# Kernel tuning notes

Measured on AMD Instinct MI355X. Metric: run time of the kernel, lower is better.

The kernel has to match this reference:

```python
import jax, jax.numpy as jnp
import numpy as np

B, T, D = 2, 4096, 512
H = 8  # heads; head_dim = D // H = 64


def setup_inputs() -> dict:
    key = jax.random.key(0)
    ks = jax.random.split(key, 8)
    s = 0.02
    return {
        "queries": jax.random.normal(ks[0], (B, T, D), jnp.float32),
        "keys": jax.random.normal(ks[1], (B, T, D), jnp.float32),
        "values": jax.random.normal(ks[2], (B, T, D), jnp.float32),
        "Wq": jax.random.normal(ks[3], (D, D), jnp.float32) * s,
        "Wk": jax.random.normal(ks[4], (D, D), jnp.float32) * s,
        "Wv": jax.random.normal(ks[5], (D, D), jnp.float32) * s,
        "Wo": jax.random.normal(ks[6], (D, D), jnp.float32) * s,
        "bo": jnp.zeros((D,), jnp.float32),
    }


def reference(queries, keys, values, Wq, Wk, Wv, Wo, bo):
    # pad_dim = 0 for in_dim=512, n_heads=8, so no padding needed.
    Bq, Tq, _ = queries.shape
    Ts = keys.shape[1]
    hd = D // H
    # torch Linear: x @ W.T
    q = (queries @ Wq.T).reshape(Bq, Tq, H, hd).transpose(0, 2, 1, 3)  # [B,H,T,hd]
    k = (keys @ Wk.T).reshape(Bq, Ts, H, hd).transpose(0, 2, 1, 3)
    v = (values @ Wv.T).reshape(Bq, Ts, H, hd).transpose(0, 2, 1, 3)
    attn = jnp.einsum("bhtd,bhsd->bhts", q, k) / np.sqrt(hd).astype(np.float32)
    attn = jax.nn.softmax(attn, axis=-1)  # [B,H,T,Ts]
    z = jnp.einsum("bhts,bhsd->bhtd", attn, v)
    z = z.transpose(0, 2, 1, 3).reshape(Bq, Tq, D)
    out = z @ Wo.T + bo
    return (out, attn)
```

## Files before the change

### kernel.cpp

```cpp
#include <hip/hip_runtime.h>

typedef __attribute__((ext_vector_type(8))) short bf16x8;
typedef __attribute__((ext_vector_type(8))) unsigned short u16x8;
typedef __attribute__((ext_vector_type(4))) float f32x4;
typedef __attribute__((ext_vector_type(2))) unsigned uint2v;
typedef __attribute__((ext_vector_type(4))) unsigned uint4v;

#define DEVINL __device__ __forceinline__

constexpr int TB = 2;
constexpr int TT = 4096;
constexpr int TD = 512;
constexpr int TH = 8;
constexpr int THD = 64;
constexpr int TM = TB * TT;

DEVINL unsigned short f2b(float f) {
  unsigned u = __builtin_bit_cast(unsigned, f);
  u += 0x7FFFu + ((u >> 16) & 1u);
  return (unsigned short)(u >> 16);
}

DEVINL unsigned cvtpk(float lo, float hi) {
  unsigned r;
  asm("v_cvt_pk_bf16_f32 %0, %1, %2" : "=v"(r) : "v"(lo), "v"(hi));
  return r;
}

DEVINL void lgkm_barrier() {
  asm volatile("s_waitcnt lgkmcnt(0)" ::: "memory");
  __builtin_amdgcn_s_barrier();
  __builtin_amdgcn_sched_barrier(0);
}

__global__ __launch_bounds__(256, 2)
void proj_qkv(const float* __restrict__ Xq, const float* __restrict__ Xk,
              const float* __restrict__ Xv, const float* __restrict__ Wq,
              const float* __restrict__ Wk, const float* __restrict__ Wv,
              unsigned short* __restrict__ qb, unsigned short* __restrict__ kb,
              unsigned short* __restrict__ vt)
{
  constexpr int K = TD, N = TD;
  __shared__ unsigned short As[128][72];
  __shared__ unsigned short Bs[128][72];

  const int z = blockIdx.z;
  const float* X = (z == 0) ? Xq : (z == 1) ? Xk : Xv;
  const float* W = (z == 0) ? Wq : (z == 1) ? Wk : Wv;
  unsigned short* Yb = (z == 0) ? qb : (z == 1) ? kb : vt;
  const bool TR = (z == 2);

  const int t    = threadIdx.x;
  const int lane = t & 63, w = t >> 6;
  const int fr = lane & 15, fq = lane >> 4;
  const int wr = (w >> 1) * 64, wc = (w & 1) * 64;
  const int bm = blockIdx.x * 128, bn = blockIdx.y * 128;
  const int srow = t >> 1;
  const int skh  = (t & 1) * 32;

  f32x4 acc[4][4];
  #pragma unroll
  for (int i = 0; i < 4; ++i)
    #pragma unroll
    for (int j = 0; j < 4; ++j)
      acc[i][j] = f32x4{0.f, 0.f, 0.f, 0.f};

  for (int k0 = 0; k0 < K; k0 += 64) {
    const float* srcA = X + (size_t)(bm + srow) * K + k0 + skh;
    const float* srcB = W + (size_t)(bn + srow) * K + k0 + skh;
    #pragma unroll
    for (int i = 0; i < 4; ++i) {
      float4 a0 = ((const float4*)srcA)[2 * i];
      float4 a1 = ((const float4*)srcA)[2 * i + 1];
      u16x8 oa = {f2b(a0.x), f2b(a0.y), f2b(a0.z), f2b(a0.w),
                  f2b(a1.x), f2b(a1.y), f2b(a1.z), f2b(a1.w)};
      *(u16x8*)&As[srow][skh + i * 8] = oa;
      float4 b0 = ((const float4*)srcB)[2 * i];
      float4 b1 = ((const float4*)srcB)[2 * i + 1];
      u16x8 ob = {f2b(b0.x), f2b(b0.y), f2b(b0.z), f2b(b0.w),
                  f2b(b1.x), f2b(b1.y), f2b(b1.z), f2b(b1.w)};
      *(u16x8*)&Bs[srow][skh + i * 8] = ob;
    }
    __syncthreads();
    #pragma unroll
    for (int kk = 0; kk < 2; ++kk) {
      bf16x8 af[4], bfv[4];
      #pragma unroll
      for (int i = 0; i < 4; ++i)
        af[i] = *(const bf16x8*)&As[wr + i * 16 + fr][kk * 32 + fq * 8];
      #pragma unroll
      for (int j = 0; j < 4; ++j)
        bfv[j] = *(const bf16x8*)&Bs[wc + j * 16 + fr][kk * 32 + fq * 8];
      if (TR) {
        #pragma unroll
        for (int i = 0; i < 4; ++i)
          #pragma unroll
          for (int j = 0; j < 4; ++j)
            acc[i][j] = __builtin_amdgcn_mfma_f32_16x16x32_bf16(bfv[i], af[j], acc[i][j], 0, 0, 0);
      } else {
        #pragma unroll
        for (int i = 0; i < 4; ++i)
          #pragma unroll
          for (int j = 0; j < 4; ++j)
            acc[i][j] = __builtin_amdgcn_mfma_f32_16x16x32_bf16(af[i], bfv[j], acc[i][j], 0, 0, 0);
      }
    }
    __syncthreads();
  }

  if (TR) {
    #pragma unroll
    for (int i = 0; i < 4; ++i)
      #pragma unroll
      for (int j = 0; j < 4; ++j)
        #pragma unroll
        for (int ii = 0; ii < 4; ++ii) {
          const int Nidx = bn + wc + i * 16 + fq * 4 + ii;
          const int Midx = bm + wr + j * 16 + fr;
          const int h = Nidx >> 6, dd = Nidx & (THD - 1);
          const int b = Midx >> 12, tt = Midx & (TT - 1);
          Yb[((size_t)(b * TH + h) * THD + dd) * TT + tt] = f2b(acc[i][j][ii]);
        }
  } else {
    #pragma unroll
    for (int i = 0; i < 4; ++i)
      #pragma unroll
      for (int j = 0; j < 4; ++j)
        #pragma unroll
        for (int ii = 0; ii < 4; ++ii) {
          const int gm = bm + wr + i * 16 + fq * 4 + ii;
          const int gn = bn + wc + j * 16 + fr;
          Yb[(size_t)gm * N + gn] = f2b(acc[i][j][ii]);
        }
  }
}

__global__ __launch_bounds__(256, 2)
void gemm_final(const float* __restrict__ X, const float* __restrict__ W,
                float* __restrict__ Yf, const float* __restrict__ bias)
{
  constexpr int K = TD, N = TD;
  __shared__ unsigned short As[128][72];
  __shared__ unsigned short Bs[128][72];

  const int t    = threadIdx.x;
  const int lane = t & 63, w = t >> 6;
  const int fr = lane & 15, fq = lane >> 4;
  const int wr = (w >> 1) * 64, wc = (w & 1) * 64;
  const int bm = blockIdx.x * 128, bn = blockIdx.y * 128;
  const int srow = t >> 1;
  const int skh  = (t & 1) * 32;

  f32x4 acc[4][4];
  #pragma unroll
  for (int i = 0; i < 4; ++i)
    #pragma unroll
    for (int j = 0; j < 4; ++j)
      acc[i][j] = f32x4{0.f, 0.f, 0.f, 0.f};

  for (int k0 = 0; k0 < K; k0 += 64) {
    const float* srcA = X + (size_t)(bm + srow) * K + k0 + skh;
    const float* srcB = W + (size_t)(bn + srow) * K + k0 + skh;
    #pragma unroll
    for (int i = 0; i < 4; ++i) {
      float4 a0 = ((const float4*)srcA)[2 * i];
      float4 a1 = ((const float4*)srcA)[2 * i + 1];
      u16x8 oa = {f2b(a0.x), f2b(a0.y), f2b(a0.z), f2b(a0.w),
                  f2b(a1.x), f2b(a1.y), f2b(a1.z), f2b(a1.w)};
      *(u16x8*)&As[srow][skh + i * 8] = oa;
      float4 b0 = ((const float4*)srcB)[2 * i];
      float4 b1 = ((const float4*)srcB)[2 * i + 1];
      u16x8 ob = {f2b(b0.x), f2b(b0.y), f2b(b0.z), f2b(b0.w),
                  f2b(b1.x), f2b(b1.y), f2b(b1.z), f2b(b1.w)};
      *(u16x8*)&Bs[srow][skh + i * 8] = ob;
    }
    __syncthreads();
    #pragma unroll
    for (int kk = 0; kk < 2; ++kk) {
      bf16x8 af[4], bfv[4];
      #pragma unroll
      for (int i = 0; i < 4; ++i)
        af[i] = *(const bf16x8*)&As[wr + i * 16 + fr][kk * 32 + fq * 8];
      #pragma unroll
      for (int j = 0; j < 4; ++j)
        bfv[j] = *(const bf16x8*)&Bs[wc + j * 16 + fr][kk * 32 + fq * 8];
      #pragma unroll
      for (int i = 0; i < 4; ++i)
        #pragma unroll
        for (int j = 0; j < 4; ++j)
          acc[i][j] = __builtin_amdgcn_mfma_f32_16x16x32_bf16(af[i], bfv[j], acc[i][j], 0, 0, 0);
    }
    __syncthreads();
  }

  #pragma unroll
  for (int i = 0; i < 4; ++i)
    #pragma unroll
    for (int j = 0; j < 4; ++j)
      #pragma unroll
      for (int ii = 0; ii < 4; ++ii) {
        const int gm = bm + wr + i * 16 + fq * 4 + ii;
        const int gn = bn + wc + j * 16 + fr;
        Yf[(size_t)gm * N + gn] = acc[i][j][ii] + bias[gn];
      }
}

__global__ __launch_bounds__(256, 4)
void attn_fused(const unsigned short* __restrict__ Qb,
                const unsigned short* __restrict__ Kb,
                const unsigned short* __restrict__ VTg,
                float* __restrict__ attnO, float* __restrict__ Z)
{
  __shared__ __align__(16) char smem_[36864];
  auto Ks  = (unsigned short (*)[32][72])smem_;
  auto VTs = (unsigned short (*)[64][40])(smem_ + 9216);
  auto KsW = (unsigned short (*)[2][32][72])smem_;

  const int t    = threadIdx.x;
  const int lane = t & 63, w = t >> 6;
  const int fr = lane & 15, fq = lane >> 4;

  const int d  = blockIdx.x;
  const int bh = 2 * (d & 7) + ((d >> 3) & 1);
  const int q0 = (d >> 4) * 64;
  const int b  = bh >> 3, h = bh & 7;

  const size_t rowKV  = ((size_t)(b * TT)) * TD + h * THD;
  const size_t vtBase = (size_t)bh * THD * TT;

  const int trK = t >> 3, tcK = (t & 7) * 8;
  const int trV = t >> 2, tcV = (t & 3) * 8;

  auto loadK = [&](int kv0, u16x8& r) {
    r = *(const u16x8*)(Kb + rowKV + (size_t)(kv0 + trK) * TD + tcK);
  };
  auto loadVT = [&](int kv0, u16x8& r) {
    r = *(const u16x8*)(VTg + vtBase + (size_t)trV * TT + kv0 + tcV);
  };
  auto writeK  = [&](int buf, const u16x8& r) { *(u16x8*)&Ks[buf][trK][tcK]  = r; };
  auto writeVT = [&](int buf, const u16x8& r) { *(u16x8*)&VTs[buf][trV][tcV] = r; };

  const unsigned short* qsrc = Qb + ((size_t)(b * TT + q0 + w * 16 + fr)) * TD + h * THD;
  bf16x8 aq[2];
  aq[0] = *(const bf16x8*)(qsrc + fq * 8);
  aq[1] = *(const bf16x8*)(qsrc + 32 + fq * 8);

  constexpr int KVB = 32;
  constexpr int NT = TT / KVB;
  constexpr float K2 = 0.18033688011112042f;

  u16x8 kr, vr;
  loadK(0, kr);
  loadVT(0, vr);
  writeK(0, kr);
  writeVT(0, vr);
  lgkm_barrier();

  float lsum = 0.f;
  f32x4 accz[4];
  #pragma unroll
  for (int n = 0; n < 4; ++n) accz[n] = f32x4{0.f, 0.f, 0.f, 0.f};

  for (int j = 0; j < NT; ++j) {
    const int cur = j & 1;
    if (j + 1 < NT) {
      loadK((j + 1) * KVB, kr);
      loadVT((j + 1) * KVB, vr);
    }
    f32x4 sv[2];
    __builtin_amdgcn_s_setprio(1);
    #pragma unroll
    for (int n = 0; n < 2; ++n) {
      f32x4 s = f32x4{0.f, 0.f, 0.f, 0.f};
      #pragma unroll
      for (int kk = 0; kk < 2; ++kk) {
        bf16x8 ak = *(const bf16x8*)&Ks[cur][n * 16 + fr][kk * 32 + fq * 8];
        s = __builtin_amdgcn_mfma_f32_16x16x32_bf16(ak, aq[kk], s, 0, 0, 0);
      }
      sv[n] = s;
    }
    __builtin_amdgcn_s_setprio(0);
    float p[2][4];
    #pragma unroll
    for (int n = 0; n < 2; ++n)
      #pragma unroll
      for (int i = 0; i < 4; ++i) {
        p[n][i] = __builtin_amdgcn_exp2f(sv[n][i] * K2);
        lsum += p[n][i];
      }
    uint4v pav = {cvtpk(p[0][0], p[0][1]), cvtpk(p[0][2], p[0][3]),
                  cvtpk(p[1][0], p[1][1]), cvtpk(p[1][2], p[1][3])};
    bf16x8 ap = __builtin_bit_cast(bf16x8, pav);
    __builtin_amdgcn_s_setprio(1);
    #pragma unroll
    for (int df = 0; df < 4; ++df) {
      uint2v lo = *(const uint2v*)&VTs[cur][df * 16 + fr][fq * 4];
      uint2v hi = *(const uint2v*)&VTs[cur][df * 16 + fr][16 + fq * 4];
      uint4v bvv = {lo[0], lo[1], hi[0], hi[1]};
      accz[df] = __builtin_amdgcn_mfma_f32_16x16x32_bf16(
          ap, __builtin_bit_cast(bf16x8, bvv), accz[df], 0, 0, 0);
    }
    __builtin_amdgcn_s_setprio(0);
    if (j + 1 < NT) {
      writeK(cur ^ 1, kr);
      writeVT(cur ^ 1, vr);
    }
    lgkm_barrier();
  }

  lsum += __shfl_xor(lsum, 16, 64);
  lsum += __shfl_xor(lsum, 32, 64);

  float rls[4];
  #pragma unroll
  for (int i = 0; i < 4; ++i)
    rls[i] = 1.0f / __shfl(lsum, fq * 4 + i, 64);
  const size_t zbase = ((size_t)(b * TT + q0 + w * 16 + fq * 4)) * TD + h * THD + fr;
  #pragma unroll
  for (int df = 0; df < 4; ++df)
    #pragma unroll
    for (int i = 0; i < 4; ++i)
      Z[zbase + (size_t)i * TD + df * 16] = accz[df][i] * rls[i];

  const float l2i = -__log2f(lsum);
  __syncthreads();

  const int phase = (37 * d + 32 * w) & (NT - 1);
  const int prow = lane >> 3, pcol = (lane & 7) * 8;
  u16x8 kr4[4];
  auto loadKW = [&](int kvt) {
    #pragma unroll
    for (int i = 0; i < 4; ++i)
      kr4[i] = *(const u16x8*)(Kb + rowKV +
                 (size_t)(kvt * KVB + i * 8 + prow) * TD + pcol);
  };
  auto writeKW = [&](int buf) {
    #pragma unroll
    for (int i = 0; i < 4; ++i)
      *(u16x8*)&KsW[w][buf][i * 8 + prow][pcol] = kr4[i];
  };

  loadKW(phase);
  writeKW(0);

  float* arow = attnO + ((size_t)bh * TT + q0 + w * 16 + fr) * TT + fq * 4;

  for (int jj = 0; jj < NT; ++jj) {
    const int cur = jj & 1;
    const int j = (jj + phase) & (NT - 1);
    if (jj + 1 < NT) loadKW((jj + 1 + phase) & (NT - 1));
    f32x4 sv[2];
    __builtin_amdgcn_s_setprio(1);
    #pragma unroll
    for (int n = 0; n < 2; ++n) {
      f32x4 s = f32x4{0.f, 0.f, 0.f, 0.f};
      #pragma unroll
      for (int kk = 0; kk < 2; ++kk) {
        bf16x8 ak = *(const bf16x8*)&KsW[w][cur][n * 16 + fr][kk * 32 + fq * 8];
        s = __builtin_amdgcn_mfma_f32_16x16x32_bf16(ak, aq[kk], s, 0, 0, 0);
      }
      sv[n] = s;
    }
    __builtin_amdgcn_s_setprio(0);
    #pragma unroll
    for (int n = 0; n < 2; ++n) {
      f32x4 pv4 = {__builtin_amdgcn_exp2f(fmaf(sv[n][0], K2, l2i)),
                   __builtin_amdgcn_exp2f(fmaf(sv[n][1], K2, l2i)),
                   __builtin_amdgcn_exp2f(fmaf(sv[n][2], K2, l2i)),
                   __builtin_amdgcn_exp2f(fmaf(sv[n][3], K2, l2i))};
      *(f32x4*)(arow + j * KVB + n * 16) = pv4;
    }
    if (jj + 1 < NT) writeKW(cur ^ 1);
  }
}

extern "C" void kernel_launch(void* const* d_in, const int* in_sizes, int n_in,
                              void* d_out, int out_size, void* d_ws, size_t ws_size,
                              hipStream_t stream) {
  const float* queries = (const float*)d_in[0];
  const float* keys    = (const float*)d_in[1];
  const float* values  = (const float*)d_in[2];
  const float* Wq = (const float*)d_in[3];
  const float* Wk = (const float*)d_in[4];
  const float* Wv = (const float*)d_in[5];
  const float* Wo = (const float*)d_in[6];
  const float* bo = (const float*)d_in[7];

  float* out  = (float*)d_out;
  float* attn = out + (size_t)TM * TD;

  unsigned short* qb = (unsigned short*)d_ws;
  unsigned short* kb = qb + (size_t)TM * TD;
  unsigned short* vt = kb + (size_t)TM * TD;
  float*          zf = (float*)(vt + (size_t)TM * TD);

  proj_qkv<<<dim3(TM / 128, TD / 128, 3), 256, 0, stream>>>(
      queries, keys, values, Wq, Wk, Wv, qb, kb, vt);

  attn_fused<<<dim3(1024), 256, 0, stream>>>(qb, kb, vt, attn, zf);

  gemm_final<<<dim3(TM / 128, TD / 128), 256, 0, stream>>>(zf, Wo, out, bo);
}
```

Baseline: 501.7 us.

## Fuse output projection GEMM into attention kernel via global completion counter

Drops the separate output-projection kernel and runs the Z@Wo^T GEMM inside the attention kernel. Each block bumps a global atomic counter once it has written its Z tile. The first 512 blocks then poll the counter between chunks of their attention-probability write loop and run one 128x64 GEMM tile as soon as all Z is ready, overlapping the GEMM with the bandwidth-bound attn stores. The approach relies on all 1024 blocks being co-resident (or making progress) to avoid deadlock. It also adds a memset launch, polling overhead, and chunked K reloads with full waits.

```diff
diff --git a/kernel.cpp b/kernel.cpp
--- a/kernel.cpp
+++ b/kernel.cpp
@@ -135,86 +135,21 @@
   }
 }
 
-__global__ __launch_bounds__(256, 2)
-void gemm_final(const float* __restrict__ X, const float* __restrict__ W,
-                float* __restrict__ Yf, const float* __restrict__ bias)
-{
-  constexpr int K = TD, N = TD;
-  __shared__ unsigned short As[128][72];
-  __shared__ unsigned short Bs[128][72];
-
-  const int t    = threadIdx.x;
-  const int lane = t & 63, w = t >> 6;
-  const int fr = lane & 15, fq = lane >> 4;
-  const int wr = (w >> 1) * 64, wc = (w & 1) * 64;
-  const int bm = blockIdx.x * 128, bn = blockIdx.y * 128;
-  const int srow = t >> 1;
-  const int skh  = (t & 1) * 32;
-
-  f32x4 acc[4][4];
-  #pragma unroll
-  for (int i = 0; i < 4; ++i)
-    #pragma unroll
-    for (int j = 0; j < 4; ++j)
-      acc[i][j] = f32x4{0.f, 0.f, 0.f, 0.f};
-
-  for (int k0 = 0; k0 < K; k0 += 64) {
-    const float* srcA = X + (size_t)(bm + srow) * K + k0 + skh;
-    const float* srcB = W + (size_t)(bn + srow) * K + k0 + skh;
-    #pragma unroll
-    for (int i = 0; i < 4; ++i) {
-      float4 a0 = ((const float4*)srcA)[2 * i];
-      float4 a1 = ((const float4*)srcA)[2 * i + 1];
-      u16x8 oa = {f2b(a0.x), f2b(a0.y), f2b(a0.z), f2b(a0.w),
-                  f2b(a1.x), f2b(a1.y), f2b(a1.z), f2b(a1.w)};
-      *(u16x8*)&As[srow][skh + i * 8] = oa;
-      float4 b0 = ((const float4*)srcB)[2 * i];
-      float4 b1 = ((const float4*)srcB)[2 * i + 1];
-      u16x8 ob = {f2b(b0.x), f2b(b0.y), f2b(b0.z), f2b(b0.w),
-                  f2b(b1.x), f2b(b1.y), f2b(b1.z), f2b(b1.w)};
-      *(u16x8*)&Bs[srow][skh + i * 8] = ob;
-    }
-    __syncthreads();
-    #pragma unroll
-    for (int kk = 0; kk < 2; ++kk) {
-      bf16x8 af[4], bfv[4];
-      #pragma unroll
-      for (int i = 0; i < 4; ++i)
-        af[i] = *(const bf16x8*)&As[wr + i * 16 + fr][kk * 32 + fq * 8];
-      #pragma unroll
-      for (int j = 0; j < 4; ++j)
-        bfv[j] = *(const bf16x8*)&Bs[wc + j * 16 + fr][kk * 32 + fq * 8];
-      #pragma unroll
-      for (int i = 0; i < 4; ++i)
-        #pragma unroll
-        for (int j = 0; j < 4; ++j)
-          acc[i][j] = __builtin_amdgcn_mfma_f32_16x16x32_bf16(af[i], bfv[j], acc[i][j], 0, 0, 0);
-    }
-    __syncthreads();
-  }
-
-  #pragma unroll
-  for (int i = 0; i < 4; ++i)
-    #pragma unroll
-    for (int j = 0; j < 4; ++j)
-      #pragma unroll
-      for (int ii = 0; ii < 4; ++ii) {
-        const int gm = bm + wr + i * 16 + fq * 4 + ii;
-        const int gn = bn + wc + j * 16 + fr;
-        Yf[(size_t)gm * N + gn] = acc[i][j][ii] + bias[gn];
-      }
-}
-
 __global__ __launch_bounds__(256, 4)
-void attn_fused(const unsigned short* __restrict__ Qb,
-                const unsigned short* __restrict__ Kb,
-                const unsigned short* __restrict__ VTg,
-                float* __restrict__ attnO, float* __restrict__ Z)
+void attn_gemm(const unsigned short* __restrict__ Qb,
+               const unsigned short* __restrict__ Kb,
+               const unsigned short* __restrict__ VTg,
+               float* __restrict__ attnO, float* __restrict__ Z,
+               const float* __restrict__ Wo, const float* __restrict__ bo,
+               float* __restrict__ outO, unsigned* __restrict__ counter)
 {
   __shared__ __align__(16) char smem_[36864];
+  __shared__ int smflag;
   auto Ks  = (unsigned short (*)[32][72])smem_;
   auto VTs = (unsigned short (*)[64][40])(smem_ + 9216);
   auto KsW = (unsigned short (*)[2][32][72])smem_;
+  auto GAs = (unsigned short (*)[72])smem_;
+  auto GBs = (unsigned short (*)[72])(smem_ + 18432);
 
   const int t    = threadIdx.x;
   const int lane = t & 63, w = t >> 6;
@@ -322,6 +257,73 @@
     for (int i = 0; i < 4; ++i)
       Z[zbase + (size_t)i * TD + df * 16] = accz[df][i] * rls[i];
 
+  __threadfence();
+  __syncthreads();
+  if (t == 0) atomicAdd(counter, 1u);
+
+  const bool isGemmBlock = (d < 512);
+  bool gemmDone = !isGemmBlock;
+
+  const int gm0 = (d >> 3) * 128, gn0 = (d & 7) * 64;
+  auto do_gemm = [&]() {
+    const int wr = (w >> 1) * 64, wc = (w & 1) * 32;
+    const int srow = t >> 1, skh = (t & 1) * 32;
+    const int brow = t >> 2, bkh = (t & 3) * 16;
+    f32x4 gacc[4][2];
+    #pragma unroll
+    for (int i = 0; i < 4; ++i)
+      #pragma unroll
+      for (int j = 0; j < 2; ++j)
+        gacc[i][j] = f32x4{0.f, 0.f, 0.f, 0.f};
+    for (int k0 = 0; k0 < TD; k0 += 64) {
+      const float* srcA = Z + (size_t)(gm0 + srow) * TD + k0 + skh;
+      #pragma unroll
+      for (int i = 0; i < 4; ++i) {
+        float4 a0 = ((const float4*)srcA)[2 * i];
+        float4 a1 = ((const float4*)srcA)[2 * i + 1];
+        u16x8 oa = {f2b(a0.x), f2b(a0.y), f2b(a0.z), f2b(a0.w),
+                    f2b(a1.x), f2b(a1.y), f2b(a1.z), f2b(a1.w)};
+        *(u16x8*)&GAs[srow][skh + i * 8] = oa;
+      }
+      const float* srcB = Wo + (size_t)(gn0 + brow) * TD + k0 + bkh;
+      #pragma unroll
+      for (int i = 0; i < 2; ++i) {
+        float4 b0 = ((const float4*)srcB)[2 * i];
+        float4 b1 = ((const float4*)srcB)[2 * i + 1];
+        u16x8 ob = {f2b(b0.x), f2b(b0.y), f2b(b0.z), f2b(b0.w),
+                    f2b(b1.x), f2b(b1.y), f2b(b1.z), f2b(b1.w)};
+        *(u16x8*)&GBs[brow][bkh + i * 8] = ob;
+      }
+      __syncthreads();
+      #pragma unroll
+      for (int kk = 0; kk < 2; ++kk) {
+        bf16x8 af[4], bfv[2];
+        #pragma unroll
+        for (int i = 0; i < 4; ++i)
+          af[i] = *(const bf16x8*)&GAs[wr + i * 16 + fr][kk * 32 + fq * 8];
+        #pragma unroll
+        for (int j = 0; j < 2; ++j)
+          bfv[j] = *(const bf16x8*)&GBs[wc + j * 16 + fr][kk * 32 + fq * 8];
+        #pragma unroll
+        for (int i = 0; i < 4; ++i)
+          #pragma unroll
+          for (int j = 0; j < 2; ++j)
+            gacc[i][j] = __builtin_amdgcn_mfma_f32_16x16x32_bf16(af[i], bfv[j], gacc[i][j], 0, 0, 0);
+      }
+      __syncthreads();
+    }
+    #pragma unroll
+    for (int i = 0; i < 4; ++i)
+      #pragma unroll
+      for (int j = 0; j < 2; ++j)
+        #pragma unroll
+        for (int ii = 0; ii < 4; ++ii) {
+          const int gm = gm0 + wr + i * 16 + fq * 4 + ii;
+          const int gn = gn0 + wc + j * 16 + fr;
+          outO[(size_t)gm * TD + gn] = gacc[i][j][ii] + bo[gn];
+        }
+  };
+
   const float l2i = -__log2f(lsum);
   __syncthreads();
 
@@ -340,37 +342,62 @@
       *(u16x8*)&KsW[w][buf][i * 8 + prow][pcol] = kr4[i];
   };
 
-  loadKW(phase);
-  writeKW(0);
-
   float* arow = attnO + ((size_t)bh * TT + q0 + w * 16 + fr) * TT + fq * 4;
 
-  for (int jj = 0; jj < NT; ++jj) {
-    const int cur = jj & 1;
-    const int j = (jj + phase) & (NT - 1);
-    if (jj + 1 < NT) loadKW((jj + 1 + phase) & (NT - 1));
-    f32x4 sv[2];
-    __builtin_amdgcn_s_setprio(1);
-    #pragma unroll
-    for (int n = 0; n < 2; ++n) {
-      f32x4 s = f32x4{0.f, 0.f, 0.f, 0.f};
-      #pragma unroll
-      for (int kk = 0; kk < 2; ++kk) {
-        bf16x8 ak = *(const bf16x8*)&KsW[w][cur][n * 16 + fr][kk * 32 + fq * 8];
-        s = __builtin_amdgcn_mfma_f32_16x16x32_bf16(ak, aq[kk], s, 0, 0, 0);
-      }
-      sv[n] = s;
-    }
-    __builtin_amdgcn_s_setprio(0);
-    #pragma unroll
-    for (int n = 0; n < 2; ++n) {
-      f32x4 pv4 = {__builtin_amdgcn_exp2f(fmaf(sv[n][0], K2, l2i)),
-                   __builtin_amdgcn_exp2f(fmaf(sv[n][1], K2, l2i)),
-                   __builtin_amdgcn_exp2f(fmaf(sv[n][2], K2, l2i)),
-                   __builtin_amdgcn_exp2f(fmaf(sv[n][3], K2, l2i))};
-      *(f32x4*)(arow + j * KVB + n * 16) = pv4;
-    }
-    if (jj + 1 < NT) writeKW(cur ^ 1);
+  for (int c = 0; c < 8; ++c) {
+    if (!gemmDone && c > 0) {
+      if (t == 0) smflag = (atomicAdd(counter, 0u) >= 1024u) ? 1 : 0;
+      __syncthreads();
+      if (smflag) {
+        __threadfence();
+        do_gemm();
+        gemmDone = true;
+        __syncthreads();
+      }
+    }
+    const int jj0 = c * 16;
+    loadKW((jj0 + phase) & (NT - 1));
+    asm volatile("s_waitcnt vmcnt(0)" ::: "memory");
+    writeKW(jj0 & 1);
+    for (int jj = jj0; jj < jj0 + 16; ++jj) {
+      const int cur = jj & 1;
+      const int j = (jj + phase) & (NT - 1);
+      if (jj + 1 < jj0 + 16) loadKW((jj + 1 + phase) & (NT - 1));
+      asm volatile("s_waitcnt lgkmcnt(0)" ::: "memory");
+      __builtin_amdgcn_sched_barrier(0);
+      f32x4 sv[2];
+      __builtin_amdgcn_s_setprio(1);
+      #pragma unroll
+      for (int n = 0; n < 2; ++n) {
+        f32x4 s = f32x4{0.f, 0.f, 0.f, 0.f};
+        #pragma unroll
+        for (int kk = 0; kk < 2; ++kk) {
+          bf16x8 ak = *(const bf16x8*)&KsW[w][cur][n * 16 + fr][kk * 32 + fq * 8];
+          s = __builtin_amdgcn_mfma_f32_16x16x32_bf16(ak, aq[kk], s, 0, 0, 0);
+        }
+        sv[n] = s;
+      }
+      __builtin_amdgcn_s_setprio(0);
+      #pragma unroll
+      for (int n = 0; n < 2; ++n) {
+        f32x4 pv4 = {__builtin_amdgcn_exp2f(fmaf(sv[n][0], K2, l2i)),
+                     __builtin_amdgcn_exp2f(fmaf(sv[n][1], K2, l2i)),
+                     __builtin_amdgcn_exp2f(fmaf(sv[n][2], K2, l2i)),
+                     __builtin_amdgcn_exp2f(fmaf(sv[n][3], K2, l2i))};
+        *(f32x4*)(arow + j * KVB + n * 16) = pv4;
+      }
+      if (jj + 1 < jj0 + 16) writeKW(cur ^ 1);
+    }
+  }
+
+  if (!gemmDone) {
+    if (t == 0) {
+      while (atomicAdd(counter, 0u) < 1024u) __builtin_amdgcn_s_sleep(8);
+      smflag = 1;
+    }
+    __syncthreads();
+    __threadfence();
+    do_gemm();
   }
 }
 
@@ -393,11 +420,13 @@
   unsigned short* kb = qb + (size_t)TM * TD;
   unsigned short* vt = kb + (size_t)TM * TD;
   float*          zf = (float*)(vt + (size_t)TM * TD);
+  unsigned*       counter = (unsigned*)(zf + (size_t)TM * TD);
 
   proj_qkv<<<dim3(TM / 128, TD / 128, 3), 256, 0, stream>>>(
       queries, keys, values, Wq, Wk, Wv, qb, kb, vt);
 
-  attn_fused<<<dim3(1024), 256, 0, stream>>>(qb, kb, vt, attn, zf);
-
-  gemm_final<<<dim3(TM / 128, TD / 128), 256, 0, stream>>>(zf, Wo, out, bo);
-}
+  hipMemsetAsync(counter, 0, sizeof(unsigned), stream);
+
+  attn_gemm<<<dim3(1024), 256, 0, stream>>>(qb, kb, vt, attn, zf,
+                                            Wo, bo, out, counter);
+}
```

Measured after the change: 726.8 us. +44.9%, slower.
